# Kernel tuning notes

Hardware: AMD Instinct MI355X
Metric: run time of the kernel (lower is better)

Reference implementation:

```python
import jax, jax.numpy as jnp
import numpy as np

BATCH = 8192
IN_DIM = 512
OUT_DIM = 512
GRID_SIZE = 5
SPLINE_ORDER = 3
# grid has 2*(G+K)+1 knots -> after K de Boor steps basis count = 2*G+K
N_BASES = 2 * GRID_SIZE + SPLINE_ORDER  # 13
CLAMP_EPS = 1e-4
DENOM_EPS = 1e-8


def _make_grid():
    step = 2.0 / GRID_SIZE
    g = jnp.arange(-GRID_SIZE - SPLINE_ORDER, GRID_SIZE + SPLINE_ORDER + 1, dtype=jnp.float32) * step
    return jnp.tile(g[None, :], (IN_DIM, 1))  # [in_dim, 2*(G+K)+1]


def _b_spline(x, grid):
    # x: [B, in], grid: [in, L] -> bases: [B, in, 2*G+K]
    xg = x[..., None]  # [B, in, 1]
    bases = ((xg >= grid[:, :-1]) & (xg < grid[:, 1:])).astype(x.dtype)
    for k in range(1, SPLINE_ORDER + 1):
        denom1 = grid[:, k:-1] - grid[:, :-(k + 1)] + DENOM_EPS
        left = (xg - grid[:, :-(k + 1)]) / denom1
        denom2 = grid[:, k + 1:] - grid[:, 1:-k] + DENOM_EPS
        right = (grid[:, k + 1:] - xg) / denom2
        bases = left * bases[..., :-1] + right * bases[..., 1:]
    return bases


def setup_inputs() -> dict:
    key = jax.random.key(0)
    k1, k2, k3 = jax.random.split(key, 3)
    x = jax.random.normal(k1, (BATCH, IN_DIM), dtype=jnp.float32)
    # kaiming_uniform(a=sqrt(5)) ~ U(-1/sqrt(fan_in), 1/sqrt(fan_in))
    b_c = 1.0 / np.sqrt(IN_DIM * N_BASES)
    coeffs = jax.random.uniform(k2, (OUT_DIM, IN_DIM, N_BASES), dtype=jnp.float32, minval=-b_c, maxval=b_c)
    b_w = 1.0 / np.sqrt(IN_DIM)
    base_weight = jax.random.uniform(k3, (OUT_DIM, IN_DIM), dtype=jnp.float32, minval=-b_w, maxval=b_w)
    return {"x": x, "coeffs": coeffs, "base_weight": base_weight}


def reference(x, coeffs, base_weight):
    grid = _make_grid()
    xc = jnp.clip(x, -1.0 + CLAMP_EPS, 1.0 - CLAMP_EPS)
    basis = _b_spline(xc, grid)                       # [B, in, nb]
    spline_out = jnp.einsum('oic,bic->bo', coeffs, basis)
    base_out = jax.nn.silu(x) @ base_weight.T         # F.linear(silu(x), W)
    y = spline_out + base_out + x                     # residual (in_dim == out_dim)
    return y
```

## Files before the change

### kernel.cpp

```cpp
#include <hip/hip_runtime.h>
#include <stdint.h>

typedef unsigned int u32;
typedef unsigned short u16;
typedef unsigned long long u64;
typedef __bf16 bf16x8 __attribute__((ext_vector_type(8)));
typedef float f32x4 __attribute__((ext_vector_type(4)));
typedef u32 u32x4 __attribute__((ext_vector_type(4)));

#define IN_DIM 512

__device__ __forceinline__ u16 bfr(float f) {
  __bf16 h = (__bf16)f;
  return __builtin_bit_cast(u16, h);
}
__device__ __forceinline__ u16 f2bf(float f) {
  u32 u = __builtin_bit_cast(u32, f);
  u += 0x7fffu + ((u >> 16) & 1u);
  return (u16)(u >> 16);
}
__device__ __forceinline__ u32 pk2(float a, float b) {
  return (u32)f2bf(a) | ((u32)f2bf(b) << 16);
}

__global__ void pack_b(const float* __restrict__ coeffs,
                       const float* __restrict__ bw,
                       char* __restrict__ Bp) {
  __shared__ float stage[64][56];
  const int tid = threadIdx.x;
  const int q = tid & 3, g = tid >> 2;
  const int id = blockIdx.x * 64 + g;
  const int col = id >> 7, s = id & 127;
  const float* cbase = coeffs + ((size_t)col * IN_DIM + s * 4) * 13;
#pragma unroll
  for (int j = 0; j < 3; ++j) {
    int ch = q + j * 4;
    float4 v = *(const float4*)(cbase + ch * 4);
    stage[g][ch * 4 + 0] = v.x; stage[g][ch * 4 + 1] = v.y;
    stage[g][ch * 4 + 2] = v.z; stage[g][ch * 4 + 3] = v.w;
  }
  if (q == 0) {
    float4 v = *(const float4*)(cbase + 48);
    stage[g][48] = v.x; stage[g][49] = v.y; stage[g][50] = v.z; stage[g][51] = v.w;
  }
  if (q == 1) {
    float4 v = *(const float4*)(bw + (size_t)col * IN_DIM + s * 4);
    stage[g][52] = v.x; stage[g][53] = v.y; stage[g][54] = v.z; stage[g][55] = v.w;
  }
  __syncthreads();
  const int nbp = col >> 7, cb = (col >> 4) & 7, cl = col & 15;
  char* base = Bp + (((size_t)(nbp * 128 + s) * 8 + cb) * 2) * 1024;
#pragma unroll
  for (int r = 0; r < 2; ++r) {
    int idx = q * 2 + r;
    int h = idx & 1;
    int dd = idx >> 1;
    int ks = dd >> 1;
    const float* sf = &stage[g][dd * 13];
    float w = stage[g][52 + dd];
    u16 hh[8];
#pragma unroll
    for (int c = 0; c < 8; ++c) {
      int slot = h * 8 + c;
      float v = slot < 13 ? sf[slot] : (slot < 15 ? w : 0.0f);
      hh[c] = bfr(v);
    }
    u32x4 o;
    o.x = (u32)hh[0] | ((u32)hh[1] << 16);
    o.y = (u32)hh[2] | ((u32)hh[3] << 16);
    o.z = (u32)hh[4] | ((u32)hh[5] << 16);
    o.w = (u32)hh[6] | ((u32)hh[7] << 16);
    int lanei = cl + 16 * (2 * (dd & 1) + h);
    *(u32x4*)(base + (size_t)ks * 1024 + lanei * 16) = o;
  }
}

__device__ __forceinline__ void expandA(float xv, char* rb, u32 swz, u32 k0) {
  float xc = fminf(fmaxf(xv, -0.9999f), 0.9999f);
  float tp = __fmaf_rn(xc, 2.5f, 3.0f);
  float fj = floorf(tp);
  int jl = (int)fj;
  float u = tp - fj;
  float u2 = u * u, u3 = u2 * u;
  float vv = 1.0f - u;
  float b0 = vv * vv * vv * (1.0f / 6.0f);
  float b3 = u3 * (1.0f / 6.0f);
  float b1 = __fmaf_rn(0.5f, u3, __fmaf_rn(u2, -1.0f, 2.0f / 3.0f));
  float b2 = 1.0f - b0 - b1 - b3;
  float e = __expf(-xv);
  float sg = __fdividef(xv, 1.0f + e);
  u16 sh = bfr(sg);
  float shf = __builtin_bit_cast(float, ((u32)sh) << 16);
  u16 sl = bfr(sg - shf);
  u32 pk01 = (u32)bfr(b0) | ((u32)bfr(b1) << 16);
  u32 pk23 = (u32)bfr(b2) | ((u32)bfr(b3) << 16);
  u64 v = (u64)pk01 | (((u64)pk23) << 32);
  int sstart = jl + 2;
  int qa = sstart >> 2;
  int shn = (sstart & 3) << 4;
  u64 lo = v << shn;
  u64 hi = shn ? (v >> (64 - shn)) : 0ull;
  u64 q0 = qa ? 0ull : lo;
  u64 q1 = qa ? lo : hi;
  u64 q2 = qa ? hi : 0ull;
  u64 q3 = (u64)(((u32)sh) << 16) | (((u64)(u32)sl) << 32);
  u32x4 c0, c1;
  c0.x = (u32)q0; c0.y = (u32)(q0 >> 32); c0.z = (u32)q1; c0.w = (u32)(q1 >> 32);
  c1.x = (u32)q2; c1.y = (u32)(q2 >> 32); c1.z = (u32)q3; c1.w = (u32)(q3 >> 32);
  *(u32x4*)(rb + ((k0 ^ swz) << 4)) = c0;
  *(u32x4*)(rb + (((k0 + 1u) ^ swz) << 4)) = c1;
}

__launch_bounds__(768, 3)
__global__ void kan_gemm(const float* __restrict__ x,
                         const char* __restrict__ Bp,
                         float* __restrict__ out) {
  __shared__ __align__(16) char smem[67584];

  const int tid = threadIdx.x;
  const int lane = tid & 63;
  const int wid = tid >> 6;
  const bool isC = (wid < 8);

  const int kt = wid >> 2;
  const int wm = (wid >> 1) & 1, wn = wid & 1;
  const int lrow = lane & 15, lkg = lane >> 4;

  int s0 = blockIdx.x;
  int xcd = s0 & 7;
  int nb = xcd >> 1;
  int mb = ((s0 >> 3) << 1) | (xcd & 1);

  const int te = tid & 255;
  const int erow = te >> 2;
  const int ad = te & 3;
  const u32 aswz = (u32)(erow & 7);
  const u32 ak0 = (u32)(ad * 2);
  const float* xpa = x + (size_t)(mb * 128 + erow) * IN_DIM + ad;
  const float* xpb = xpa + (size_t)64 * IN_DIM;

  const char* bptr = Bp + (((size_t)(nb * 128) * 8 + wn * 4) * 2 + kt) * 1024 + (size_t)lane * 16;

  f32x4 acc[4][4];
#pragma unroll
  for (int i = 0; i < 4; ++i)
#pragma unroll
    for (int j = 0; j < 4; ++j) acc[i][j] = (f32x4){0.f, 0.f, 0.f, 0.f};

  u32x4 bA[4], bB[4];
  char* r0 = smem;
  char* r1 = smem + 16384;
  char* r2 = smem + 32768;

  float xa1 = 0.f, xa2 = 0.f, xb1 = 0.f, xb2 = 0.f;
  if (isC) {
#pragma unroll
    for (int fn = 0; fn < 4; ++fn)
      bA[fn] = *(const u32x4*)(bptr + fn * 2048);
  } else {
    expandA(xpa[0], r0 + erow * 128, aswz, ak0);
    expandA(xpb[0], r0 + (erow + 64) * 128, aswz, ak0);
    expandA(xpa[4], r1 + erow * 128, aswz, ak0);
    expandA(xpb[4], r1 + (erow + 64) * 128, aswz, ak0);
    xa1 = xpa[8];  xb1 = xpb[8];
    xa2 = xpa[12]; xb2 = xpb[12];
  }
  __syncthreads();

  const u32 asl = (((u32)(kt * 4) | (u32)lkg) ^ (u32)(lrow & 7)) << 4;

#define STEP(S, RB, WB, BCUR, BNXT)                                            \
  {                                                                            \
    if (isC) {                                                                 \
      bf16x8 af[4];                                                            \
      const char* arb = (RB) + (wm * 64 + lrow) * 128;                         \
      _Pragma("unroll")                                                        \
      for (int fm = 0; fm < 4; ++fm)                                           \
        af[fm] = __builtin_bit_cast(bf16x8,                                    \
            *(const u32x4*)(arb + fm * 2048 + asl));                           \
      int sl_ = (S) + 1 < 128 ? (S) + 1 : 127;                                 \
      _Pragma("unroll")                                                        \
      for (int fn = 0; fn < 4; ++fn)                                           \
        BNXT[fn] = *(const u32x4*)(bptr + (size_t)sl_ * 16384 + fn * 2048);    \
      __builtin_amdgcn_s_setprio(1);                                           \
      _Pragma("unroll")                                                        \
      for (int fm = 0; fm < 4; ++fm)                                           \
        _Pragma("unroll")                                                      \
        for (int fn = 0; fn < 4; ++fn)                                         \
          acc[fm][fn] = __builtin_amdgcn_mfma_f32_16x16x32_bf16(               \
              af[fm], __builtin_bit_cast(bf16x8, BCUR[fn]), acc[fm][fn],       \
              0, 0, 0);                                                        \
      __builtin_amdgcn_s_setprio(0);                                           \
    } else {                                                                   \
      if ((S) + 2 < 128) {                                                     \
        expandA(xa1, (WB) + erow * 128, aswz, ak0);                            \
        expandA(xb1, (WB) + (erow + 64) * 128, aswz, ak0);                     \
      }                                                                        \
      int xi = ((S) + 4 < 128 ? (S) + 4 : 127) * 4;                            \
      float na = xpa[xi], nbv = xpb[xi];                                       \
      xa1 = xa2; xa2 = na; xb1 = xb2; xb2 = nbv;                               \
      asm volatile("s_waitcnt lgkmcnt(0)" ::: "memory");                       \
    }                                                                          \
    __builtin_amdgcn_s_barrier();                                              \
  }

#pragma unroll 1
  for (int s = 0; s < 128; s += 2) {
    STEP(s, r0, r2, bA, bB)
    STEP(s + 1, r1, r0, bB, bA)
    char* t = r2; r2 = r1; r1 = r0; r0 = t;
  }

  __syncthreads();

  float* red = (float*)smem;
  if (isC && kt == 1) {
#pragma unroll
    for (int fm = 0; fm < 4; ++fm)
#pragma unroll
      for (int fn = 0; fn < 4; ++fn) {
        int rr = wm * 64 + fm * 16 + lkg * 4;
        int cc = wn * 64 + fn * 16 + lrow;
#pragma unroll
        for (int r = 0; r < 4; ++r)
          red[(size_t)(rr + r) * 132 + cc] = acc[fm][fn][r];
      }
  }
  __syncthreads();
  if (isC && kt == 0) {
#pragma unroll
    for (int fm = 0; fm < 4; ++fm)
#pragma unroll
      for (int fn = 0; fn < 4; ++fn) {
        int rr = wm * 64 + fm * 16 + lkg * 4;
        int cc = wn * 64 + fn * 16 + lrow;
        size_t gb = (size_t)(mb * 128 + rr) * IN_DIM + nb * 128 + cc;
#pragma unroll
        for (int r = 0; r < 4; ++r) {
          size_t off = gb + (size_t)r * IN_DIM;
          out[off] = acc[fm][fn][r] + red[(size_t)(rr + r) * 132 + cc] + x[off];
        }
      }
  }
}

__device__ __forceinline__ void st_b16(char* rb, u32 swz, u32 k0, int c, u16 v) {
  u32 uc = (u32)c;
  u32 byte = (((k0 + (uc >> 3)) ^ swz) << 4) | ((uc & 7u) << 1);
  *(u16*)(rb + byte) = v;
}

__device__ __forceinline__ void stage_a_fb(char* aT, int row, int d, float xv) {
  char* rb = aT + row * 128;
  u32 swz = (u32)(row & 7);
  float xc = fminf(fmaxf(xv, -0.9999f), 0.9999f);
  float tp = __fmaf_rn(xc, 2.5f, 3.0f);
  float fj = floorf(tp);
  int jl = (int)fj;
  float u = tp - fj;
  float u2 = u * u, u3 = u2 * u;
  float vv = 1.0f - u;
  float b0 = vv * vv * vv * (1.0f / 6.0f);
  float b3 = u3 * (1.0f / 6.0f);
  float b1 = __fmaf_rn(0.5f, u3, __fmaf_rn(u2, -1.0f, 2.0f / 3.0f));
  float b2 = 1.0f - b0 - b1 - b3;
  float e = __expf(-xv);
  float sg = __fdividef(xv, 1.0f + e);
  u16 sh = f2bf(sg);
  float shf = __builtin_bit_cast(float, ((u32)sh) << 16);
  u16 slo = f2bf(sg - shf);
  u32 k0 = (u32)d * 2u;
  u32x4 z = {0u, 0u, 0u, 0u};
  *(u32x4*)(rb + ((k0 ^ swz) << 4)) = z;
  u32x4 z2 = {0u, 0u, ((u32)sh) << 16, (u32)slo};
  *(u32x4*)(rb + (((k0 + 1u) ^ swz) << 4)) = z2;
  st_b16(rb, swz, k0, jl + 2, f2bf(b0));
  st_b16(rb, swz, k0, jl + 3, f2bf(b1));
  st_b16(rb, swz, k0, jl + 4, f2bf(b2));
  st_b16(rb, swz, k0, jl + 5, f2bf(b3));
}

__launch_bounds__(512, 2)
__global__ void kan_fused(const float* __restrict__ x,
                          const float* __restrict__ coeffs,
                          const float* __restrict__ bw,
                          float* __restrict__ out) {
  __shared__ __align__(16) char smem[65536];
  const int tid = threadIdx.x;
  const int lane = tid & 63;
  const int wid = tid >> 6;
  const int team = wid >> 2;
  const int wm = (wid >> 1) & 1;
  const int wn = wid & 1;
  const int m0 = wm * 64, n0 = wn * 64;
  const int lrow = lane & 15;
  const int lkg = lane >> 4;
  int s = blockIdx.x;
  int xcd = s & 7;
  int nb = xcd >> 1;
  int mb = (s >> 3) | ((xcd & 1) << 5);
  const int t = tid & 255;
  const int arow = t >> 1;
  const int h = t & 1;
  char* aT = smem + team * 16384;
  char* bT = smem + 32768 + team * 16384;
  const int dim0 = team * 256;
  const float* xptr = x + (size_t)(mb * 128 + arow) * IN_DIM + dim0 + 2 * h;
  const float* cptr = coeffs + ((size_t)((nb * 128 + arow) * IN_DIM) + dim0) * 13 + 26 * h;
  const float* wptr = bw + (size_t)(nb * 128 + arow) * IN_DIM + dim0 + 2 * h;
  f32x4 acc[4][4];
#pragma unroll
  for (int i = 0; i < 4; ++i)
#pragma unroll
    for (int j = 0; j < 4; ++j) acc[i][j] = (f32x4){0.f, 0.f, 0.f, 0.f};
  float2 xv, wv;
  float2 cv0, cv1, cv2, cv3, cv4, cv5, cv6, cv7, cv8, cv9, cv10, cv11, cv12;
#define PREFETCH(STP)                                                     \
  {                                                                       \
    const float* cp_ = cptr + (STP) * 52;                                 \
    xv = *(const float2*)(xptr + (STP) * 4);                              \
    wv = *(const float2*)(wptr + (STP) * 4);                              \
    cv0 = *(const float2*)(cp_ + 0);   cv1 = *(const float2*)(cp_ + 2);   \
    cv2 = *(const float2*)(cp_ + 4);   cv3 = *(const float2*)(cp_ + 6);   \
    cv4 = *(const float2*)(cp_ + 8);   cv5 = *(const float2*)(cp_ + 10);  \
    cv6 = *(const float2*)(cp_ + 12);  cv7 = *(const float2*)(cp_ + 14);  \
    cv8 = *(const float2*)(cp_ + 16);  cv9 = *(const float2*)(cp_ + 18);  \
    cv10 = *(const float2*)(cp_ + 20); cv11 = *(const float2*)(cp_ + 22); \
    cv12 = *(const float2*)(cp_ + 24);                                    \
  }
  PREFETCH(0)
  for (int st = 0; st < 64; ++st) {
    stage_a_fb(aT, arow, 2 * h + 0, xv.x);
    stage_a_fb(aT, arow, 2 * h + 1, xv.y);
    {
      char* rb = bT + arow * 128;
      u32 swz = (u32)(arow & 7);
      u32 k0 = (u32)(2 * h) * 2u;
      u32x4 lo, hi;
      lo.x = pk2(cv0.x, cv0.y); lo.y = pk2(cv1.x, cv1.y);
      lo.z = pk2(cv2.x, cv2.y); lo.w = pk2(cv3.x, cv3.y);
      hi.x = pk2(cv4.x, cv4.y); hi.y = pk2(cv5.x, cv5.y);
      {
        u16 wb = f2bf(wv.x);
        hi.z = (u32)f2bf(cv6.x) | ((u32)wb << 16);
        hi.w = (u32)wb;
      }
      *(u32x4*)(rb + ((k0 ^ swz) << 4)) = lo;
      *(u32x4*)(rb + (((k0 + 1u) ^ swz) << 4)) = hi;
      lo.x = pk2(cv6.y, cv7.x);  lo.y = pk2(cv7.y, cv8.x);
      lo.z = pk2(cv8.y, cv9.x);  lo.w = pk2(cv9.y, cv10.x);
      hi.x = pk2(cv10.y, cv11.x); hi.y = pk2(cv11.y, cv12.x);
      {
        u16 wb = f2bf(wv.y);
        hi.z = (u32)f2bf(cv12.y) | ((u32)wb << 16);
        hi.w = (u32)wb;
      }
      *(u32x4*)(rb + (((k0 + 2u) ^ swz) << 4)) = lo;
      *(u32x4*)(rb + (((k0 + 3u) ^ swz) << 4)) = hi;
    }
    __syncthreads();
    if (st != 63) { PREFETCH(st + 1) }
    {
      const char* arb = aT + (m0 + lrow) * 128;
      const char* brb = bT + (n0 + lrow) * 128;
      u32 rsw = (u32)(lrow & 7);
#pragma unroll
      for (int ks = 0; ks < 2; ++ks) {
        u32 sl2 = (((u32)(ks * 4) | (u32)lkg) ^ rsw) << 4;
        bf16x8 af[4], bfr2[4];
#pragma unroll
        for (int fm = 0; fm < 4; ++fm)
          af[fm] = __builtin_bit_cast(bf16x8, *(const u32x4*)(arb + fm * 2048 + sl2));
#pragma unroll
        for (int fn = 0; fn < 4; ++fn)
          bfr2[fn] = __builtin_bit_cast(bf16x8, *(const u32x4*)(brb + fn * 2048 + sl2));
#pragma unroll
        for (int fm = 0; fm < 4; ++fm)
#pragma unroll
          for (int fn = 0; fn < 4; ++fn)
            acc[fm][fn] = __builtin_amdgcn_mfma_f32_16x16x32_bf16(
                af[fm], bfr2[fn], acc[fm][fn], 0, 0, 0);
      }
    }
    __syncthreads();
  }
  float* red = (float*)smem;
  if (team == 1) {
#pragma unroll
    for (int fm = 0; fm < 4; ++fm)
#pragma unroll
      for (int fn = 0; fn < 4; ++fn) {
        int rr = m0 + fm * 16 + lkg * 4;
        int cc = n0 + fn * 16 + lrow;
#pragma unroll
        for (int r = 0; r < 4; ++r) red[(rr + r) * 128 + cc] = acc[fm][fn][r];
      }
  }
  __syncthreads();
  if (team == 0) {
#pragma unroll
    for (int fm = 0; fm < 4; ++fm)
#pragma unroll
      for (int fn = 0; fn < 4; ++fn) {
        int rr = m0 + fm * 16 + lkg * 4;
        int ccol = n0 + fn * 16 + lrow;
        int grow = mb * 128 + rr;
        int gcol = nb * 128 + ccol;
#pragma unroll
        for (int r = 0; r < 4; ++r) {
          float v = acc[fm][fn][r] + red[(rr + r) * 128 + ccol] +
                    x[(size_t)(grow + r) * IN_DIM + gcol];
          out[(size_t)(grow + r) * IN_DIM + gcol] = v;
        }
      }
  }
}

extern "C" void kernel_launch(void* const* d_in, const int* in_sizes, int n_in,
                              void* d_out, int out_size, void* d_ws, size_t ws_size,
                              hipStream_t stream) {
  const float* x = (const float*)d_in[0];
  const float* coeffs = (const float*)d_in[1];
  const float* bw = (const float*)d_in[2];
  float* out = (float*)d_out;
  if (ws_size >= (size_t)512 * 16384) {
    char* Bp = (char*)d_ws;
    hipLaunchKernelGGL(pack_b, dim3(1024), dim3(256), 0, stream, coeffs, bw, Bp);
    hipLaunchKernelGGL(kan_gemm, dim3(256), dim3(768), 0, stream, x, Bp, out);
  } else {
    hipLaunchKernelGGL(kan_fused, dim3(256), dim3(512), 0, stream, x, coeffs, bw, out);
  }
}
```

Measured before the change: 99.69 us.

## Stage x tiles into LDS via async global_load_lds triple buffering

The expander waves no longer issue scattered scalar global loads of x each step. They prefetch 32-column chunks of x straight into a triple-buffered, swizzled LDS region using global_load_lds, two chunks ahead, and read the values back from LDS for the basis expansion. This aims to replace strided 4-byte global loads with coalesced 16-byte async copies and take their latency off the critical path. LDS use grows from about 66KB to 96KB per block, which may reduce how many blocks fit per CU under the launch bounds of 3.

```diff
diff --git a/kernel.cpp b/kernel.cpp
--- a/kernel.cpp
+++ b/kernel.cpp
@@ -22,6 +22,10 @@
 __device__ __forceinline__ u32 pk2(float a, float b) {
   return (u32)f2bf(a) | ((u32)f2bf(b) << 16);
 }
+
+#define GLDS(G, L) \
+  __builtin_amdgcn_global_load_lds((const __attribute__((address_space(1))) u32*)(G), \
+                                   (__attribute__((address_space(3))) u32*)(L), 16, 0, 0)
 
 __global__ void pack_b(const float* __restrict__ coeffs,
                        const float* __restrict__ bw,
@@ -115,7 +119,7 @@
 __global__ void kan_gemm(const float* __restrict__ x,
                          const char* __restrict__ Bp,
                          float* __restrict__ out) {
-  __shared__ __align__(16) char smem[67584];
+  __shared__ __align__(16) char smem[98304];
 
   const int tid = threadIdx.x;
   const int lane = tid & 63;
@@ -139,6 +143,12 @@
   const float* xpa = x + (size_t)(mb * 128 + erow) * IN_DIM + ad;
   const float* xpb = xpa + (size_t)64 * IN_DIM;
 
+  char* xs = smem + 49152;
+  const int ew = wid - 8;
+  const int grb = mb * 128 + ew * 32 + (lane >> 3);
+  const int g2 = (lane & 7) ^ (lane >> 3);
+  const u32 xrd = (u32)(ad * 4);
+
   const char* bptr = Bp + (((size_t)(nb * 128) * 8 + wn * 4) * 2 + kt) * 1024 + (size_t)lane * 16;
 
   f32x4 acc[4][4];
@@ -152,18 +162,22 @@
   char* r1 = smem + 16384;
   char* r2 = smem + 32768;
 
-  float xa1 = 0.f, xa2 = 0.f, xb1 = 0.f, xb2 = 0.f;
   if (isC) {
 #pragma unroll
     for (int fn = 0; fn < 4; ++fn)
       bA[fn] = *(const u32x4*)(bptr + fn * 2048);
   } else {
+#pragma unroll
+    for (int c = 0; c < 2; ++c)
+#pragma unroll
+      for (int k = 0; k < 4; ++k) {
+        const float* ga = x + (size_t)(grb + k * 8) * IN_DIM + c * 32 + g2 * 4;
+        GLDS(ga, xs + c * 16384 + ((ew * 4 + k) << 10));
+      }
     expandA(xpa[0], r0 + erow * 128, aswz, ak0);
     expandA(xpb[0], r0 + (erow + 64) * 128, aswz, ak0);
     expandA(xpa[4], r1 + erow * 128, aswz, ak0);
     expandA(xpb[4], r1 + (erow + 64) * 128, aswz, ak0);
-    xa1 = xpa[8];  xb1 = xpb[8];
-    xa2 = xpa[12]; xb2 = xpb[12];
   }
   __syncthreads();
 
@@ -192,13 +206,30 @@
               0, 0, 0);                                                        \
       __builtin_amdgcn_s_setprio(0);                                           \
     } else {                                                                   \
+      if (((S) & 7) == 0) {                                                    \
+        int c2 = ((S) >> 3) + 2;                                               \
+        if (c2 < 16) {                                                         \
+          char* xdst = xs + (c2 % 3) * 16384;                                  \
+          _Pragma("unroll")                                                    \
+          for (int k = 0; k < 4; ++k) {                                        \
+            const float* ga = x + (size_t)(grb + k * 8) * IN_DIM + c2 * 32 + g2 * 4; \
+            GLDS(ga, xdst + ((ew * 4 + k) << 10));                             \
+          }                                                                    \
+          asm volatile("s_waitcnt vmcnt(4)" ::: "memory");                     \
+        } else {                                                               \
+          asm volatile("s_waitcnt vmcnt(0)" ::: "memory");                     \
+        }                                                                      \
+      }                                                                        \
       if ((S) + 2 < 128) {                                                     \
-        expandA(xa1, (WB) + erow * 128, aswz, ak0);                            \
-        expandA(xb1, (WB) + (erow + 64) * 128, aswz, ak0);                     \
+        int Sp = (S) + 2;                                                      \
+        int cc = Sp >> 3, gg = Sp & 7;                                         \
+        const char* xb_ = xs + (cc % 3) * 16384;                               \
+        u32 xo = ((u32)(gg ^ (erow & 7)) << 4) + xrd;                          \
+        float xa = *(const float*)(xb_ + erow * 128 + xo);                     \
+        float xv2 = *(const float*)(xb_ + (erow + 64) * 128 + xo);             \
+        expandA(xa, (WB) + erow * 128, aswz, ak0);                             \
+        expandA(xv2, (WB) + (erow + 64) * 128, aswz, ak0);                     \
       }                                                                        \
-      int xi = ((S) + 4 < 128 ? (S) + 4 : 127) * 4;                            \
-      float na = xpa[xi], nbv = xpb[xi];                                       \
-      xa1 = xa2; xa2 = na; xb1 = xb2; xb2 = nbv;                               \
       asm volatile("s_waitcnt lgkmcnt(0)" ::: "memory");                       \
     }                                                                          \
     __builtin_amdgcn_s_barrier();                                              \
```

Measured after the change: 112.8 us. 13.1% more time.
